# Performance work log

Hardware: AMD Instinct MI355X
Metric: run time of the kernel (lower is better)

The kernel has to match this reference:

```python
import jax, jax.numpy as jnp
import numpy as np

N = 4096        # num nodes
D = 512         # d_model (in_dim)
F = 512         # dff (out_dim)
H = 4           # num_heads
ALPHA = 0.3     # tf.keras LeakyReLU default


def setup_inputs() -> dict:
    key = jax.random.key(0)
    ks = jax.random.split(key, 9)
    s_in = 1.0 / np.sqrt(D)
    s_out = 1.0 / np.sqrt(F)
    return {
        "nodes": jax.random.normal(ks[0], (N, D), jnp.float32),
        "edges": jax.random.normal(ks[1], (N, D), jnp.float32),
        "labels": jax.random.normal(ks[2], (N, D), jnp.float32),
        # edge_layer Dense(dff)
        "We": jax.random.normal(ks[3], (D, F), jnp.float32) * s_in,
        "be": jnp.zeros((F,), jnp.float32),
        # per-head kernels stacked on leading head axis
        "W": jax.random.normal(ks[4], (H, D, F), jnp.float32) * s_in,
        "b": jax.random.normal(ks[5], (H, F), jnp.float32) * 0.01,
        "u": jax.random.normal(ks[6], (H, F), jnp.float32) * s_out,  # attn_kernel_self (squeezed)
        "v": jax.random.normal(ks[7], (H, F), jnp.float32) * s_out,  # attn_kernel_neighs (squeezed)
    }


def reference(nodes, edges, labels, We, be, W, b, u, v):
    # edge projection shared across heads: Dense(edges + labels)
    e = (edges + labels) @ We + be                       # [N, F]
    # per-head node projection: features = nodes @ W_h + b_h
    feats = jnp.einsum('nd,hdf->hnf', nodes, W) + b[:, None, :]   # [H, N, F]
    # rank-1 additive attention scores
    a_self = jnp.einsum('hnf,hf->hn', feats, u)          # [H, N]
    a_neigh = jnp.einsum('hnf,hf->hn', feats, v)         # [H, N]
    feats = feats + e[None]                              # [H, N, F]
    scores = a_self[:, :, None] * a_neigh[:, None, :]    # [H, N, N] outer product
    scores = jnp.where(scores >= 0, scores, ALPHA * scores)  # LeakyReLU(0.3)
    attn = jax.nn.softmax(scores, axis=-1)               # [H, N, N]
    out = jnp.einsum('hnm,hmf->hnf', attn, feats)        # [H, N, F]
    return jax.nn.relu(out.mean(axis=0))                 # [N, F]
```

## Files before the change

### kernel.cpp

```cpp
#include <hip/hip_runtime.h>

#define NN 4096
#define DD 512
#define FF 512
#define HH 4

typedef _Float16 f16;
typedef f16 f16x8 __attribute__((ext_vector_type(8)));
typedef f16 f16x4 __attribute__((ext_vector_type(4)));
typedef float f32x4 __attribute__((ext_vector_type(4)));

typedef __attribute__((address_space(1))) void gvoid;
typedef __attribute__((address_space(3))) void svoid;
__device__ __forceinline__ void glds16(const void* g, void* s) {
    __builtin_amdgcn_global_load_lds((gvoid*)g, (svoid*)s, 16, 0, 0);
}

__device__ __attribute__((aligned(16))) f16 g_nodesH[NN * DD];
__device__ __attribute__((aligned(16))) f16 g_XH[NN * DD];
__device__ __attribute__((aligned(16))) f16 g_WeTH[FF * DD];
__device__ __attribute__((aligned(16))) f16 g_WTH[HH * FF * DD];
__device__ __attribute__((aligned(16))) f16 g_eH[FF * NN];
__device__ __attribute__((aligned(16))) f16 g_featsH[HH * FF * NN];
__device__ __attribute__((aligned(16))) f16 g_oaccH[(size_t)2 * HH * NN * FF];
__device__ float g_beF[FF];
__device__ float g_bF[HH * FF];
__device__ float g_tu[HH * DD], g_tv[HH * DD], g_bu[HH], g_bv[HH];
__device__ float g_p[HH * NN], g_q[HH * NN], g_M[HH * NN], g_sc[HH * NN];

#define PREP_CONV 16394
#define PREP_TRAN 320
#define PREP_UV   513

__global__ __launch_bounds__(256) void k_prep(const float* __restrict__ nodes, const float* __restrict__ edges,
                                              const float* __restrict__ labels, const float* __restrict__ We,
                                              const float* __restrict__ W, const float* __restrict__ be,
                                              const float* __restrict__ b, const float* __restrict__ u,
                                              const float* __restrict__ v) {
    __shared__ float lds[64 * 65];
    int bx = blockIdx.x;
    int tid = threadIdx.x;
    if (bx < PREP_CONV) {
        int id = bx * 256 + tid;
        const int NDE = NN * DD;
        if (id < NDE) { g_nodesH[id] = (f16)nodes[id]; return; }
        id -= NDE;
        if (id < NDE) { g_XH[id] = (f16)(edges[id] + labels[id]); return; }
        id -= NDE;
        if (id < FF) { g_beF[id] = be[id]; return; }
        id -= FF;
        if (id < HH * FF) { g_bF[id] = b[id]; return; }
        return;
    }
    if (bx < PREP_CONV + PREP_TRAN) {
        int bid = bx - PREP_CONV;
        int mi = bid >> 6;
        int t64 = bid & 63;
        const float* src = (mi == 0) ? We : (W + (size_t)(mi - 1) * DD * FF);
        f16* dst = (mi == 0) ? g_WeTH : (g_WTH + (size_t)(mi - 1) * FF * DD);
        int ti = t64 >> 3, tj = t64 & 7;
        int r = tid >> 2, cseg = (tid & 3) * 16;
#pragma unroll
        for (int kq = 0; kq < 4; ++kq) {
            f32x4 vv = *(const f32x4*)(src + (size_t)(ti * 64 + r) * 512 + tj * 64 + cseg + kq * 4);
            *(f32x4*)&lds[r * 65 + cseg + kq * 4] = vv;
        }
        __syncthreads();
        int fl = tid >> 2, dseg = (tid & 3) * 16;
        f16x8 o0, o1;
#pragma unroll
        for (int k = 0; k < 8; ++k) o0[k] = (f16)lds[(dseg + k) * 65 + fl];
#pragma unroll
        for (int k = 0; k < 8; ++k) o1[k] = (f16)lds[(dseg + 8 + k) * 65 + fl];
        size_t ob = (size_t)(tj * 64 + fl) * 512 + ti * 64 + dseg;
        *(f16x8*)&dst[ob] = o0;
        *(f16x8*)&dst[ob + 8] = o1;
        return;
    }
    {
        int row = (bx - PREP_CONV - PREP_TRAN) * 4 + (tid >> 6);
        int lane = tid & 63;
        float su = 0.f, sv = 0.f;
        if (row < HH * DD) {
            int h = row >> 9, d = row & 511;
            size_t wb = (size_t)h * DD * FF + (size_t)d * FF;
#pragma unroll
            for (int j = 0; j < 8; ++j) {
                int f = lane + 64 * j;
                float wv = W[wb + f];
                su += wv * u[(size_t)h * FF + f];
                sv += wv * v[(size_t)h * FF + f];
            }
        } else if (row < HH * DD + HH) {
            int h = row - HH * DD;
#pragma unroll
            for (int j = 0; j < 8; ++j) {
                int f = lane + 64 * j;
                float bvv = b[(size_t)h * FF + f];
                su += bvv * u[(size_t)h * FF + f];
                sv += bvv * v[(size_t)h * FF + f];
            }
        }
#pragma unroll
        for (int m = 1; m < 64; m <<= 1) {
            su += __shfl_xor(su, m, 64);
            sv += __shfl_xor(sv, m, 64);
        }
        if (lane == 0 && row < HH * DD + HH) {
            if (row < HH * DD) { g_tu[row] = su; g_tv[row] = sv; }
            else { g_bu[row - HH * DD] = su; g_bv[row - HH * DD] = sv; }
        }
    }
}

__global__ __launch_bounds__(256) void k_pq() {
    int row = blockIdx.x * 4 + (threadIdx.x >> 6);
    int lane = threadIdx.x & 63;
    int h = row >> 12, n = row & 4095;
    const f16* nb = g_nodesH + (size_t)n * DD;
    const float* tu = g_tu + h * DD;
    const float* tv = g_tv + h * DD;
    float pa = 0.f, qa = 0.f;
#pragma unroll
    for (int j = 0; j < 8; ++j) {
        int d = lane + 64 * j;
        float nv = (float)nb[d];
        pa += nv * tu[d];
        qa += nv * tv[d];
    }
#pragma unroll
    for (int m = 1; m < 64; m <<= 1) {
        pa += __shfl_xor(pa, m, 64);
        qa += __shfl_xor(qa, m, 64);
    }
    if (lane == 0) {
        g_p[row] = pa + g_bu[h];
        g_q[row] = qa + g_bv[h];
    }
}

__global__ __launch_bounds__(256, 2) void k_gemm_e() {
    __shared__ f16 As[128 * 64];
    __shared__ f16 Bs[128 * 64];
    int tid = threadIdx.x;
    int lane = tid & 63, wave = tid >> 6;
    int wr = wave & 1, wf = wave >> 1;
    int c = lane & 15, g = lane >> 4;
    int n0 = blockIdx.x * 128, f0 = blockIdx.y * 128;
    int r8 = lane >> 3;
    int ksw = ((lane & 7) ^ r8) * 8;
    f32x4 acc[4][4] = {};
    for (int kk = 0; kk < DD; kk += 64) {
        __syncthreads();
#pragma unroll
        for (int j = 0; j < 4; ++j) {
            int row = wave * 32 + j * 8;
            glds16(g_XH   + (size_t)(n0 + row + r8) * DD + kk + ksw, &As[row * 64]);
            glds16(g_WeTH + (size_t)(f0 + row + r8) * DD + kk + ksw, &Bs[row * 64]);
        }
        __syncthreads();
#pragma unroll
        for (int s = 0; s < 2; ++s) {
            f16x8 af[4], bf[4];
#pragma unroll
            for (int i = 0; i < 4; ++i)
                af[i] = *(const f16x8*)&As[(wr * 64 + i * 16 + c) * 64 + (((s * 4 + g) ^ (c & 7)) * 8)];
#pragma unroll
            for (int jj = 0; jj < 4; ++jj)
                bf[jj] = *(const f16x8*)&Bs[(wf * 64 + jj * 16 + c) * 64 + (((s * 4 + g) ^ (c & 7)) * 8)];
#pragma unroll
            for (int i = 0; i < 4; ++i)
#pragma unroll
                for (int jj = 0; jj < 4; ++jj)
                    acc[i][jj] = __builtin_amdgcn_mfma_f32_16x16x32_f16(af[i], bf[jj], acc[i][jj], 0, 0, 0);
        }
    }
#pragma unroll
    for (int jj = 0; jj < 4; ++jj) {
        int f = f0 + wf * 64 + jj * 16 + c;
        float bv = g_beF[f];
#pragma unroll
        for (int i = 0; i < 4; ++i) {
            int r0 = n0 + wr * 64 + i * 16 + g * 4;
            f16x4 ov;
#pragma unroll
            for (int rr = 0; rr < 4; ++rr) ov[rr] = (f16)(acc[i][jj][rr] + bv);
            *(f16x4*)(g_eH + (size_t)f * NN + r0) = ov;
        }
    }
}

__global__ __launch_bounds__(256, 2) void k_gemm_feats() {
    __shared__ f16 As[128 * 64];
    __shared__ f16 Bs[128 * 64];
    int tid = threadIdx.x;
    int lane = tid & 63, wave = tid >> 6;
    int wr = wave & 1, wf = wave >> 1;
    int c = lane & 15, g = lane >> 4;
    int n0 = blockIdx.x * 128, f0 = blockIdx.y * 128;
    int h = blockIdx.z;
    const f16* Bgl = g_WTH + (size_t)h * DD * FF;
    int r8 = lane >> 3;
    int ksw = ((lane & 7) ^ r8) * 8;
    f32x4 acc[4][4] = {};
    for (int kk = 0; kk < DD; kk += 64) {
        __syncthreads();
#pragma unroll
        for (int j = 0; j < 4; ++j) {
            int row = wave * 32 + j * 8;
            glds16(g_nodesH + (size_t)(n0 + row + r8) * DD + kk + ksw, &As[row * 64]);
            glds16(Bgl      + (size_t)(f0 + row + r8) * DD + kk + ksw, &Bs[row * 64]);
        }
        __syncthreads();
#pragma unroll
        for (int s = 0; s < 2; ++s) {
            f16x8 af[4], bf[4];
#pragma unroll
            for (int i = 0; i < 4; ++i)
                af[i] = *(const f16x8*)&As[(wr * 64 + i * 16 + c) * 64 + (((s * 4 + g) ^ (c & 7)) * 8)];
#pragma unroll
            for (int jj = 0; jj < 4; ++jj)
                bf[jj] = *(const f16x8*)&Bs[(wf * 64 + jj * 16 + c) * 64 + (((s * 4 + g) ^ (c & 7)) * 8)];
#pragma unroll
            for (int i = 0; i < 4; ++i)
#pragma unroll
                for (int jj = 0; jj < 4; ++jj)
                    acc[i][jj] = __builtin_amdgcn_mfma_f32_16x16x32_f16(af[i], bf[jj], acc[i][jj], 0, 0, 0);
        }
    }
#pragma unroll
    for (int jj = 0; jj < 4; ++jj) {
        int f = f0 + wf * 64 + jj * 16 + c;
        float bv = g_bF[h * FF + f];
#pragma unroll
        for (int i = 0; i < 4; ++i) {
            int r0 = n0 + wr * 64 + i * 16 + g * 4;
            f16x4 e4 = *(const f16x4*)(g_eH + (size_t)f * NN + r0);
            f16x4 ov;
#pragma unroll
            for (int rr = 0; rr < 4; ++rr)
                ov[rr] = (f16)(acc[i][jj][rr] + bv + (float)e4[rr]);
            *(f16x4*)(g_featsH + ((size_t)h * FF + f) * NN + r0) = ov;
        }
    }
}

__global__ __launch_bounds__(256) void k_msz() {
    __shared__ float qsh[NN];
    __shared__ float red[256];
    int h = blockIdx.y;
    int tid = threadIdx.x;
    float lmax = -1e30f, lmin = 1e30f;
    for (int i = tid; i < NN; i += 256) {
        float qv = g_q[h * NN + i];
        qsh[i] = qv;
        lmax = fmaxf(lmax, qv);
        lmin = fminf(lmin, qv);
    }
    red[tid] = lmax;
    __syncthreads();
    for (int s = 128; s > 0; s >>= 1) {
        if (tid < s) red[tid] = fmaxf(red[tid], red[tid + s]);
        __syncthreads();
    }
    float qmax = red[0];
    __syncthreads();
    red[tid] = lmin;
    __syncthreads();
    for (int s = 128; s > 0; s >>= 1) {
        if (tid < s) red[tid] = fminf(red[tid], red[tid + s]);
        __syncthreads();
    }
    float qmin = red[0];
    __syncthreads();
    int nl = tid & 15, chunk = tid >> 4;
    int n = blockIdx.x * 16 + nl;
    float pv = g_p[h * NN + n];
    float se = pv * (pv >= 0.f ? qmax : qmin);
    float M = fmaxf(se, 0.3f * se);
    float z = 0.f;
    int base = chunk * 256;
    for (int i = 0; i < 64; ++i) {
        f32x4 qv = *(const f32x4*)&qsh[base + i * 4];
#pragma unroll
        for (int k = 0; k < 4; ++k) {
            float s = pv * qv[k];
            s = fmaxf(s, 0.3f * s);
            z += __expf(s - M);
        }
    }
    red[chunk * 16 + nl] = z;
    __syncthreads();
    if (chunk == 0) {
        float Z = 0.f;
#pragma unroll
        for (int t = 0; t < 16; ++t) Z += red[t * 16 + nl];
        g_M[h * NN + n] = M;
        g_sc[h * NN + n] = 0.25f / Z;
    }
}

#define ALD 68
__global__ __launch_bounds__(512, 2) void k_gemm_out() {
    __shared__ f16 As[128 * ALD];
    __shared__ f16 BsL[512 * 32];
    __shared__ f16 BsH[512 * 32];
    int tid = threadIdx.x;
    int lane = tid & 63, wave = tid >> 6;
    int wr = wave & 1;
    int wf = wave >> 1;
    int c = lane & 15, g = lane >> 4;
    int n0 = blockIdx.x * 128;
    int h = blockIdx.y;
    int ks = blockIdx.z;
    int wn = tid >> 2, kq = (tid & 3) * 16;
    float pv = g_p[h * NN + n0 + wn];
    float mv = g_M[h * NN + n0 + wn];
    float sv = g_sc[h * NN + n0 + wn];
    const float* qh = g_q + h * NN + ks * 2048;
    const f16* Bgl = g_featsH + (size_t)h * FF * NN + (size_t)ks * 2048;
    int brow = lane >> 2;
    int bksw = ((lane & 3) ^ (brow & 3)) * 8;
    f32x4 acc[4][8] = {};
    for (int kk = 0; kk < 2048; kk += 64) {
        f16x8 w0, w1;
#pragma unroll
        for (int half = 0; half < 2; ++half) {
            f32x4 qa = *(const f32x4*)(qh + kk + kq + half * 8);
            f32x4 qb = *(const f32x4*)(qh + kk + kq + half * 8 + 4);
#pragma unroll
            for (int k = 0; k < 4; ++k) {
                float s = pv * qa[k];
                s = fmaxf(s, 0.3f * s);
                if (half == 0) w0[k] = (f16)(__expf(s - mv) * sv);
                else           w1[k] = (f16)(__expf(s - mv) * sv);
            }
#pragma unroll
            for (int k = 0; k < 4; ++k) {
                float s = pv * qb[k];
                s = fmaxf(s, 0.3f * s);
                if (half == 0) w0[4 + k] = (f16)(__expf(s - mv) * sv);
                else           w1[4 + k] = (f16)(__expf(s - mv) * sv);
            }
        }
        __syncthreads();
        *(f16x8*)&As[wn * ALD + kq] = w0;
        *(f16x8*)&As[wn * ALD + kq + 8] = w1;
#pragma unroll
        for (int j = 0; j < 4; ++j) {
            int frow = wave * 64 + j * 16;
            glds16(Bgl + (size_t)(frow + brow) * NN + kk + bksw,      &BsL[frow * 32]);
            glds16(Bgl + (size_t)(frow + brow) * NN + kk + 32 + bksw, &BsH[frow * 32]);
        }
        __syncthreads();
#pragma unroll
        for (int s = 0; s < 2; ++s) {
            const f16* Bsrc = (s == 0) ? BsL : BsH;
            f16x8 af[4], bfr[8];
#pragma unroll
            for (int i = 0; i < 4; ++i)
                af[i] = *(const f16x8*)&As[(wr * 64 + i * 16 + c) * ALD + s * 32 + g * 8];
#pragma unroll
            for (int jj = 0; jj < 8; ++jj)
                bfr[jj] = *(const f16x8*)&Bsrc[(wf * 128 + jj * 16 + c) * 32 + ((g ^ (c & 3)) * 8)];
#pragma unroll
            for (int i = 0; i < 4; ++i)
#pragma unroll
                for (int jj = 0; jj < 8; ++jj)
                    acc[i][jj] = __builtin_amdgcn_mfma_f32_16x16x32_f16(af[i], bfr[jj], acc[i][jj], 0, 0, 0);
        }
    }
    f16* O = g_oaccH + (size_t)(h * 2 + ks) * NN * FF;
#pragma unroll
    for (int jj = 0; jj < 8; ++jj) {
        int f = wf * 128 + jj * 16 + c;
#pragma unroll
        for (int i = 0; i < 4; ++i) {
            int r0 = n0 + wr * 64 + i * 16 + g * 4;
#pragma unroll
            for (int rr = 0; rr < 4; ++rr)
                O[(size_t)(r0 + rr) * FF + f] = (f16)acc[i][jj][rr];
        }
    }
}

__global__ void k_reduce(float* __restrict__ out) {
    size_t i = ((size_t)blockIdx.x * 256 + threadIdx.x) * 4;
    const size_t NF = (size_t)NN * FF;
    f32x4 s = {0.f, 0.f, 0.f, 0.f};
#pragma unroll
    for (int sl = 0; sl < 8; ++sl) {
        f16x4 v = *(const f16x4*)(g_oaccH + sl * NF + i);
#pragma unroll
        for (int rr = 0; rr < 4; ++rr) s[rr] += (float)v[rr];
    }
    f32x4 o;
#pragma unroll
    for (int rr = 0; rr < 4; ++rr) o[rr] = fmaxf(s[rr], 0.f);
    *(f32x4*)(out + i) = o;
}

extern "C" void kernel_launch(void* const* d_in, const int* in_sizes, int n_in,
                              void* d_out, int out_size, void* d_ws, size_t ws_size,
                              hipStream_t stream) {
    (void)in_sizes; (void)n_in; (void)out_size; (void)d_ws; (void)ws_size;
    const float* nodes  = (const float*)d_in[0];
    const float* edges  = (const float*)d_in[1];
    const float* labels = (const float*)d_in[2];
    const float* We     = (const float*)d_in[3];
    const float* be     = (const float*)d_in[4];
    const float* W      = (const float*)d_in[5];
    const float* b      = (const float*)d_in[6];
    const float* u      = (const float*)d_in[7];
    const float* v      = (const float*)d_in[8];

    k_prep<<<PREP_CONV + PREP_TRAN + PREP_UV, 256, 0, stream>>>(nodes, edges, labels, We, W, be, b, u, v);
    k_pq<<<4096, 256, 0, stream>>>();
    k_gemm_e<<<dim3(32, 4), 256, 0, stream>>>();
    k_gemm_feats<<<dim3(32, 4, 4), 256, 0, stream>>>();
    k_msz<<<dim3(256, 4), 256, 0, stream>>>();
    k_gemm_out<<<dim3(32, 4, 2), 512, 0, stream>>>();
    k_reduce<<<2048, 256, 0, stream>>>((float*)d_out);
}
```

Before: 266.4 us.

## Fold edge projection into per-head feats GEMM via concatenated K dimension

Concatenates nodes and (edges+labels) along K into one [N,1024] operand, with W_h and We stacked per head into a [H,F,1024] operand, so a single GEMM computes feats+e directly. Removes the separate e GEMM kernel, its launch, and the e buffer write and re-read in the feats epilogue. In exchange the e projection is recomputed once per head (the edge half of the FLOPs is repeated four times), and We is written four times during prep.

```diff
diff --git a/kernel.cpp b/kernel.cpp
--- a/kernel.cpp
+++ b/kernel.cpp
@@ -4,6 +4,7 @@
 #define DD 512
 #define FF 512
 #define HH 4
+#define KK 1024
 
 typedef _Float16 f16;
 typedef f16 f16x8 __attribute__((ext_vector_type(8)));
@@ -16,19 +17,15 @@
     __builtin_amdgcn_global_load_lds((gvoid*)g, (svoid*)s, 16, 0, 0);
 }
 
-__device__ __attribute__((aligned(16))) f16 g_nodesH[NN * DD];
-__device__ __attribute__((aligned(16))) f16 g_XH[NN * DD];
-__device__ __attribute__((aligned(16))) f16 g_WeTH[FF * DD];
-__device__ __attribute__((aligned(16))) f16 g_WTH[HH * FF * DD];
-__device__ __attribute__((aligned(16))) f16 g_eH[FF * NN];
+__device__ __attribute__((aligned(16))) f16 g_catA[NN * KK];
+__device__ __attribute__((aligned(16))) f16 g_catB[HH * FF * KK];
 __device__ __attribute__((aligned(16))) f16 g_featsH[HH * FF * NN];
 __device__ __attribute__((aligned(16))) f16 g_oaccH[(size_t)2 * HH * NN * FF];
-__device__ float g_beF[FF];
-__device__ float g_bF[HH * FF];
+__device__ float g_bcat[HH * FF];
 __device__ float g_tu[HH * DD], g_tv[HH * DD], g_bu[HH], g_bv[HH];
 __device__ float g_p[HH * NN], g_q[HH * NN], g_M[HH * NN], g_sc[HH * NN];
 
-#define PREP_CONV 16394
+#define PREP_CONV 16392
 #define PREP_TRAN 320
 #define PREP_UV   513
 
@@ -43,13 +40,17 @@
     if (bx < PREP_CONV) {
         int id = bx * 256 + tid;
         const int NDE = NN * DD;
-        if (id < NDE) { g_nodesH[id] = (f16)nodes[id]; return; }
+        if (id < NDE) {
+            g_catA[(size_t)(id >> 9) * KK + (id & 511)] = (f16)nodes[id];
+            return;
+        }
         id -= NDE;
-        if (id < NDE) { g_XH[id] = (f16)(edges[id] + labels[id]); return; }
+        if (id < NDE) {
+            g_catA[(size_t)(id >> 9) * KK + 512 + (id & 511)] = (f16)(edges[id] + labels[id]);
+            return;
+        }
         id -= NDE;
-        if (id < FF) { g_beF[id] = be[id]; return; }
-        id -= FF;
-        if (id < HH * FF) { g_bF[id] = b[id]; return; }
+        if (id < HH * FF) { g_bcat[id] = b[id] + be[id & 511]; return; }
         return;
     }
     if (bx < PREP_CONV + PREP_TRAN) {
@@ -57,7 +58,6 @@
         int mi = bid >> 6;
         int t64 = bid & 63;
         const float* src = (mi == 0) ? We : (W + (size_t)(mi - 1) * DD * FF);
-        f16* dst = (mi == 0) ? g_WeTH : (g_WTH + (size_t)(mi - 1) * FF * DD);
         int ti = t64 >> 3, tj = t64 & 7;
         int r = tid >> 2, cseg = (tid & 3) * 16;
 #pragma unroll
@@ -72,9 +72,20 @@
         for (int k = 0; k < 8; ++k) o0[k] = (f16)lds[(dseg + k) * 65 + fl];
 #pragma unroll
         for (int k = 0; k < 8; ++k) o1[k] = (f16)lds[(dseg + 8 + k) * 65 + fl];
-        size_t ob = (size_t)(tj * 64 + fl) * 512 + ti * 64 + dseg;
-        *(f16x8*)&dst[ob] = o0;
-        *(f16x8*)&dst[ob + 8] = o1;
+        size_t frow = (size_t)(tj * 64 + fl);
+        size_t dcol = (size_t)(ti * 64 + dseg);
+        if (mi == 0) {
+#pragma unroll
+            for (int hh = 0; hh < HH; ++hh) {
+                size_t ob = ((size_t)hh * FF + frow) * KK + 512 + dcol;
+                *(f16x8*)&g_catB[ob] = o0;
+                *(f16x8*)&g_catB[ob + 8] = o1;
+            }
+        } else {
+            size_t ob = ((size_t)(mi - 1) * FF + frow) * KK + dcol;
+            *(f16x8*)&g_catB[ob] = o0;
+            *(f16x8*)&g_catB[ob + 8] = o1;
+        }
         return;
     }
     {
@@ -117,7 +128,7 @@
     int row = blockIdx.x * 4 + (threadIdx.x >> 6);
     int lane = threadIdx.x & 63;
     int h = row >> 12, n = row & 4095;
-    const f16* nb = g_nodesH + (size_t)n * DD;
+    const f16* nb = g_catA + (size_t)n * KK;
     const float* tu = g_tu + h * DD;
     const float* tv = g_tv + h * DD;
     float pa = 0.f, qa = 0.f;
@@ -136,57 +147,6 @@
     if (lane == 0) {
         g_p[row] = pa + g_bu[h];
         g_q[row] = qa + g_bv[h];
-    }
-}
-
-__global__ __launch_bounds__(256, 2) void k_gemm_e() {
-    __shared__ f16 As[128 * 64];
-    __shared__ f16 Bs[128 * 64];
-    int tid = threadIdx.x;
-    int lane = tid & 63, wave = tid >> 6;
-    int wr = wave & 1, wf = wave >> 1;
-    int c = lane & 15, g = lane >> 4;
-    int n0 = blockIdx.x * 128, f0 = blockIdx.y * 128;
-    int r8 = lane >> 3;
-    int ksw = ((lane & 7) ^ r8) * 8;
-    f32x4 acc[4][4] = {};
-    for (int kk = 0; kk < DD; kk += 64) {
-        __syncthreads();
-#pragma unroll
-        for (int j = 0; j < 4; ++j) {
-            int row = wave * 32 + j * 8;
-            glds16(g_XH   + (size_t)(n0 + row + r8) * DD + kk + ksw, &As[row * 64]);
-            glds16(g_WeTH + (size_t)(f0 + row + r8) * DD + kk + ksw, &Bs[row * 64]);
-        }
-        __syncthreads();
-#pragma unroll
-        for (int s = 0; s < 2; ++s) {
-            f16x8 af[4], bf[4];
-#pragma unroll
-            for (int i = 0; i < 4; ++i)
-                af[i] = *(const f16x8*)&As[(wr * 64 + i * 16 + c) * 64 + (((s * 4 + g) ^ (c & 7)) * 8)];
-#pragma unroll
-            for (int jj = 0; jj < 4; ++jj)
-                bf[jj] = *(const f16x8*)&Bs[(wf * 64 + jj * 16 + c) * 64 + (((s * 4 + g) ^ (c & 7)) * 8)];
-#pragma unroll
-            for (int i = 0; i < 4; ++i)
-#pragma unroll
-                for (int jj = 0; jj < 4; ++jj)
-                    acc[i][jj] = __builtin_amdgcn_mfma_f32_16x16x32_f16(af[i], bf[jj], acc[i][jj], 0, 0, 0);
-        }
-    }
-#pragma unroll
-    for (int jj = 0; jj < 4; ++jj) {
-        int f = f0 + wf * 64 + jj * 16 + c;
-        float bv = g_beF[f];
-#pragma unroll
-        for (int i = 0; i < 4; ++i) {
-            int r0 = n0 + wr * 64 + i * 16 + g * 4;
-            f16x4 ov;
-#pragma unroll
-            for (int rr = 0; rr < 4; ++rr) ov[rr] = (f16)(acc[i][jj][rr] + bv);
-            *(f16x4*)(g_eH + (size_t)f * NN + r0) = ov;
-        }
     }
 }
 
@@ -199,17 +159,17 @@
     int c = lane & 15, g = lane >> 4;
     int n0 = blockIdx.x * 128, f0 = blockIdx.y * 128;
     int h = blockIdx.z;
-    const f16* Bgl = g_WTH + (size_t)h * DD * FF;
+    const f16* Bgl = g_catB + (size_t)h * FF * KK;
     int r8 = lane >> 3;
     int ksw = ((lane & 7) ^ r8) * 8;
     f32x4 acc[4][4] = {};
-    for (int kk = 0; kk < DD; kk += 64) {
+    for (int kk = 0; kk < KK; kk += 64) {
         __syncthreads();
 #pragma unroll
         for (int j = 0; j < 4; ++j) {
             int row = wave * 32 + j * 8;
-            glds16(g_nodesH + (size_t)(n0 + row + r8) * DD + kk + ksw, &As[row * 64]);
-            glds16(Bgl      + (size_t)(f0 + row + r8) * DD + kk + ksw, &Bs[row * 64]);
+            glds16(g_catA + (size_t)(n0 + row + r8) * KK + kk + ksw, &As[row * 64]);
+            glds16(Bgl    + (size_t)(f0 + row + r8) * KK + kk + ksw, &Bs[row * 64]);
         }
         __syncthreads();
 #pragma unroll
@@ -231,15 +191,13 @@
 #pragma unroll
     for (int jj = 0; jj < 4; ++jj) {
         int f = f0 + wf * 64 + jj * 16 + c;
-        float bv = g_bF[h * FF + f];
+        float bv = g_bcat[h * FF + f];
 #pragma unroll
         for (int i = 0; i < 4; ++i) {
             int r0 = n0 + wr * 64 + i * 16 + g * 4;
-            f16x4 e4 = *(const f16x4*)(g_eH + (size_t)f * NN + r0);
             f16x4 ov;
 #pragma unroll
-            for (int rr = 0; rr < 4; ++rr)
-                ov[rr] = (f16)(acc[i][jj][rr] + bv + (float)e4[rr]);
+            for (int rr = 0; rr < 4; ++rr) ov[rr] = (f16)(acc[i][jj][rr] + bv);
             *(f16x4*)(g_featsH + ((size_t)h * FF + f) * NN + r0) = ov;
         }
     }
@@ -416,7 +374,6 @@
 
     k_prep<<<PREP_CONV + PREP_TRAN + PREP_UV, 256, 0, stream>>>(nodes, edges, labels, We, W, be, b, u, v);
     k_pq<<<4096, 256, 0, stream>>>();
-    k_gemm_e<<<dim3(32, 4), 256, 0, stream>>>();
     k_gemm_feats<<<dim3(32, 4, 4), 256, 0, stream>>>();
     k_msz<<<dim3(256, 4), 256, 0, stream>>>();
     k_gemm_out<<<dim3(32, 4, 2), 512, 0, stream>>>();
```

New measurement: 260.4 us. -2.3%, faster.
